# Kernel optimization log

Measured on AMD Instinct MI355X. Metric: run time of the kernel, lower is better.

The kernel has to match this reference:

```python
import jax, jax.numpy as jnp
import numpy as np

# 20 amino-acid letters and per-residue atom counts (len(struct.atoms) - 1 in the source)
LETTERS = "ARNDCQEGHILKMFPSTWYV"
RES_LEN = {"A": 4, "R": 10, "N": 7, "D": 7, "C": 5, "Q": 8, "E": 8, "G": 3, "H": 9,
           "I": 7, "L": 7, "K": 8, "M": 7, "F": 10, "P": 6, "S": 5, "T": 6, "W": 13,
           "Y": 11, "V": 6}
BATCH = 16
N_RES = 1024       # number of residues (output 'nodes')
ATOM_DIM = 64
AMINO_DIM = 256
INDS = 1           # one trailing (3,) tensor axis


def make_metadata():
    """Deterministic protein sequence + per-letter gather indices (static numpy)."""
    rng = np.random.default_rng(42)
    seq = rng.integers(0, len(LETTERS), size=N_RES)
    lens = np.array([RES_LEN[LETTERS[s]] for s in seq])
    starts = np.concatenate([[0], np.cumsum(lens)[:-1]])  # residue_indices
    atoms = int(lens.sum())
    # group residues by letter: (residue positions, atom gather indices (n_l, L))
    groups = {}
    for li, letter in enumerate(LETTERS):
        pos = np.where(seq == li)[0]
        if len(pos) == 0:
            continue
        L = RES_LEN[letter]
        idx = starts[pos][:, None] + np.arange(L)[None, :]  # (n_l, L)
        groups[letter] = (pos, idx)
    # static row offsets of each letter's weight block inside the flat weight
    offsets, off = {}, 0
    for letter in LETTERS:
        offsets[letter] = off
        off += RES_LEN[letter] * ATOM_DIM
    return atoms, groups, offsets


def setup_inputs() -> dict:
    atoms, groups, offsets = make_metadata()
    key = jax.random.key(0)
    k1, k2 = jax.random.split(key)
    x = jax.random.normal(k1, (BATCH, atoms, ATOM_DIM, 3), dtype=jnp.float32)
    total_rows = sum(RES_LEN[l] for l in LETTERS) * ATOM_DIM  # 147*64 = 9408
    W = jax.random.normal(k2, (total_rows, AMINO_DIM), dtype=jnp.float32)
    # per-expert 1/sqrt(fan_in) init scaling
    scale = np.zeros((total_rows, 1), np.float32)
    for l in LETTERS:
        fan = RES_LEN[l] * ATOM_DIM
        scale[offsets[l]:offsets[l] + fan] = 1.0 / np.sqrt(fan)
    W = W * jnp.asarray(scale)
    return {"x": x, "W_flat": W}


def reference(x, W_flat):
    """x: (B, atoms, D, 3); W_flat: (sum_l L_l*D, amino_dim).
    Equivalent to per-residue slice -> reshape -> per-letter TensLinear -> stack,
    but grouped by letter into batched GEMMs (same math, reordered)."""
    atoms, groups, offsets = make_metadata()
    B = x.shape[0]
    out = jnp.zeros((B, N_RES, AMINO_DIM, 3), dtype=x.dtype)
    for letter, (pos, idx) in groups.items():  # fixed loop over <=20 expert types
        L = RES_LEN[letter]
        fan = L * ATOM_DIM
        g = x[:, idx]                              # (B, n_l, L, D, 3) gather
        g = g.reshape(B, len(pos), fan, 3)         # flatten residue atoms x channels
        Wl = W_flat[offsets[letter]:offsets[letter] + fan]  # (fan, amino_dim)
        y = jnp.einsum("bnki,ko->bnoi", g, Wl)     # (B, n_l, amino_dim, 3)
        out = out.at[:, pos].set(y)                # scatter back into residue order
    return out
```

## Files before the change

### kernel.cpp

```cpp
#include <hip/hip_runtime.h>
#include <hip/hip_bf16.h>
#include <cstdint>
#include <cstddef>

#define NRES 1024
#define NB 16
#define ADIM 64
#define ODIM 256
#define TOTROWS 9408

typedef __bf16 bf16x8 __attribute__((ext_vector_type(8)));
typedef float f32x4 __attribute__((ext_vector_type(4)));

struct Meta {
    uint16_t start[NRES];
    uint8_t  letter[NRES];
    int atoms;
};

constexpr int RES_LEN_A[20] = {4,10,7,7,5,8,8,3,9,7,7,8,7,10,6,5,6,13,11,6};

constexpr uint32_t ss_hash(uint32_t value, uint32_t& hc) {
    value ^= hc;
    hc *= 0x931e8875u;
    value *= hc;
    value ^= value >> 16;
    return value;
}
constexpr uint32_t ss_mix(uint32_t x, uint32_t y) {
    uint32_t r = 0xca01f9ddu * x - 0x4973f715u * y;
    r ^= r >> 16;
    return r;
}

constexpr Meta make_meta() {
    Meta m = {};
    uint32_t pool[4] = {0,0,0,0};
    uint32_t hc = 0x43b0d7e5u;
    pool[0] = ss_hash(42u, hc);
    pool[1] = ss_hash(0u, hc);
    pool[2] = ss_hash(0u, hc);
    pool[3] = ss_hash(0u, hc);
    for (int s = 0; s < 4; ++s)
        for (int d = 0; d < 4; ++d)
            if (s != d) pool[d] = ss_mix(pool[d], ss_hash(pool[s], hc));
    uint32_t hb = 0x8b51f9ddu;
    uint64_t w[8] = {};
    for (int i = 0; i < 8; ++i) {
        uint32_t dv = pool[i & 3] ^ hb;
        hb *= 0x58f38dedu;
        dv *= hb;
        dv ^= dv >> 16;
        w[i] = dv;
    }
    uint64_t s64[4] = {};
    for (int i = 0; i < 4; ++i) s64[i] = w[2*i] | (w[2*i+1] << 32);
    using u128 = unsigned __int128;
    const u128 MULT = ((u128)2549297995355413924ULL << 64) | (u128)4865540595714422341ULL;
    u128 initstate = ((u128)s64[0] << 64) | (u128)s64[1];
    u128 initseq   = ((u128)s64[2] << 64) | (u128)s64[3];
    u128 inc = (initseq << 1) | (u128)1;
    u128 state = inc;
    state += initstate;
    state = state * MULT + inc;
    bool has32 = false;
    uint32_t cached = 0;
    int atoms = 0;
    for (int i = 0; i < NRES; ++i) {
        uint32_t res = 0;
        while (true) {
            uint32_t r32;
            if (has32) { r32 = cached; has32 = false; }
            else {
                state = state * MULT + inc;
                uint64_t hi = (uint64_t)(state >> 64);
                uint64_t lo = (uint64_t)state;
                uint32_t rot = (uint32_t)(state >> 122);
                uint64_t v = hi ^ lo;
                uint64_t o64 = (v >> rot) | (v << ((64u - rot) & 63u));
                cached = (uint32_t)(o64 >> 32);
                has32 = true;
                r32 = (uint32_t)o64;
            }
            uint64_t mm = (uint64_t)r32 * 20ull;
            uint32_t leftover = (uint32_t)mm;
            if (leftover >= 16u) { res = (uint32_t)(mm >> 32); break; }
        }
        m.letter[i] = (uint8_t)res;
        m.start[i] = (uint16_t)atoms;
        atoms += RES_LEN_A[res];
    }
    m.atoms = atoms;
    return m;
}

constexpr Meta H_META = make_meta();

struct LetterTab {
    int woff[21];
    int fan[20];
};
constexpr LetterTab make_tab() {
    LetterTab t = {};
    int off = 0;
    for (int l = 0; l < 20; ++l) {
        t.woff[l] = off;
        t.fan[l] = RES_LEN_A[l] * ADIM;
        off += t.fan[l];
    }
    t.woff[20] = off;
    return t;
}

struct Perm { uint16_t p[NRES]; };
constexpr Perm make_perm() {
    int ord[20];
    for (int i = 0; i < 20; ++i) ord[i] = i;
    for (int a = 0; a < 20; ++a) {
        int best = a;
        for (int j = a + 1; j < 20; ++j)
            if (RES_LEN_A[ord[j]] > RES_LEN_A[ord[best]]) best = j;
        int t = ord[a]; ord[a] = ord[best]; ord[best] = t;
    }
    Perm pr = {};
    int n = 0;
    for (int oi = 0; oi < 20; ++oi) {
        const int l = ord[oi];
        for (int p = 0; p < NRES; ++p)
            if (H_META.letter[p] == l) pr.p[n++] = (uint16_t)p;
    }
    return pr;
}

__constant__ Meta g_meta = make_meta();
__constant__ LetterTab g_tab = make_tab();
__constant__ Perm g_perm = make_perm();

__device__ __bf16 g_Wt[(size_t)TOTROWS * ODIM];

__global__ __launch_bounds__(256) void prep_W_kernel(const float* __restrict__ W) {
    const int tid = threadIdx.x;
    const int b = blockIdx.x * 4 + (tid >> 6);
    const int lane = tid & 63;
    const int l15 = lane & 15;
    const int g4 = lane >> 4;

    int l = 0;
    while (b >= (g_tab.woff[l + 1] >> 1)) ++l;
    const int rel = b - (g_tab.woff[l] >> 1);
    const int c = rel >> 5;
    const int r32 = rel & 31;
    const int h = r32 >> 4;
    const int wv = (r32 >> 2) & 3;
    const int nt = r32 & 3;

    const int n = wv * 64 + nt * 16 + l15;
    const int kg = g_tab.woff[l] + c * 64 + h * 32 + g4 * 8;

    bf16x8 v;
    #pragma unroll
    for (int q = 0; q < 8; ++q)
        v[q] = (__bf16)W[(size_t)(kg + q) * ODIM + n];
    *(bf16x8*)&g_Wt[(size_t)b * 512 + (size_t)(l15 * 4 + g4) * 8] = v;
}

__global__ __launch_bounds__(256) void lin_mfma_kernel(const float* __restrict__ x,
                                                       float* __restrict__ out,
                                                       int atoms) {
    const int p = g_perm.p[blockIdx.x];
    const int letter = g_meta.letter[p];
    const int start = g_meta.start[p];
    const int fan = g_tab.fan[letter];
    const __bf16* wslab = g_Wt + (size_t)g_tab.woff[letter] * ODIM;

    const int tid = threadIdx.x;
    const int lane = tid & 63;
    const int wv = tid >> 6;
    const int l15 = lane & 15;
    const int g4 = lane >> 4;

    __shared__ __align__(16) __bf16 As[2][48][72];

    const float* xb = x + (size_t)start * 192;
    const size_t bstr = (size_t)atoms * 192;
    const int nc = fan >> 6;

    int bl_[3], r4_[3];
    #pragma unroll
    for (int j = 0; j < 3; ++j) {
        const int e4 = tid + 256 * j;
        bl_[j] = e4 / 48;
        r4_[j] = e4 - bl_[j] * 48;
    }

    f32x4 acc[3][4];
    #pragma unroll
    for (int t = 0; t < 3; ++t)
        #pragma unroll
        for (int nt = 0; nt < 4; ++nt)
            acc[t][nt] = (f32x4){0.f, 0.f, 0.f, 0.f};

    float4 sa0, sa1, sa2;
    float4 sb0, sb1, sb2;

    auto LOADX = [&](int cc, float4& v0, float4& v1, float4& v2) {
        const size_t koff = (size_t)cc * 192;
        v0 = *(const float4*)&xb[(size_t)bl_[0] * bstr + koff + (size_t)r4_[0] * 4];
        v1 = *(const float4*)&xb[(size_t)bl_[1] * bstr + koff + (size_t)r4_[1] * 4];
        v2 = *(const float4*)&xb[(size_t)bl_[2] * bstr + koff + (size_t)r4_[2] * 4];
    };

    auto CHUNK = [&](int buf, int cc, float4& v0, float4& v1, float4& v2) {
        const float4 vv[3] = {v0, v1, v2};
        #pragma unroll
        for (int j = 0; j < 3; ++j) {
            const float f[4] = {vv[j].x, vv[j].y, vv[j].z, vv[j].w};
            #pragma unroll
            for (int q = 0; q < 4; ++q) {
                const int r = r4_[j] * 4 + q;
                const int kl = r / 3, i = r - kl * 3;
                As[buf][bl_[j] * 3 + i][kl] = (__bf16)f[q];
            }
        }
        if (cc + 2 < nc) LOADX(cc + 2, v0, v1, v2);
        __syncthreads();

        const __bf16* wchunk = wslab + (size_t)cc * 16384 + (size_t)wv * 2048
                             + (size_t)(l15 * 4 + g4) * 8;
        #pragma unroll
        for (int h = 0; h < 2; ++h) {
            bf16x8 a[3], wf[4];
            #pragma unroll
            for (int t = 0; t < 3; ++t)
                a[t] = *(const bf16x8*)&As[buf][t * 16 + l15][h * 32 + g4 * 8];
            #pragma unroll
            for (int nt = 0; nt < 4; ++nt)
                wf[nt] = *(const bf16x8*)(wchunk + (size_t)h * 8192 + (size_t)nt * 512);
            #pragma unroll
            for (int nt = 0; nt < 4; ++nt)
                #pragma unroll
                for (int t = 0; t < 3; ++t)
                    acc[t][nt] = __builtin_amdgcn_mfma_f32_16x16x32_bf16(a[t], wf[nt], acc[t][nt], 0, 0, 0);
        }
    };

    LOADX(0, sa0, sa1, sa2);
    LOADX(1, sb0, sb1, sb2);
    int c = 0;
    while (true) {
        CHUNK(c & 1, c, sa0, sa1, sa2);
        if (++c == nc) break;
        CHUNK(c & 1, c, sb0, sb1, sb2);
        if (++c == nc) break;
    }

    #pragma unroll
    for (int t = 0; t < 3; ++t)
        #pragma unroll
        for (int reg = 0; reg < 4; ++reg) {
            const int r = t * 16 + g4 * 4 + reg;
            const int bl = r / 3;
            const int i = r - bl * 3;
            #pragma unroll
            for (int nt = 0; nt < 4; ++nt) {
                const int o = wv * 64 + nt * 16 + l15;
                out[(((size_t)bl * NRES + p) * ODIM + o) * 3 + i] = acc[t][nt][reg];
            }
        }
}

extern "C" void kernel_launch(void* const* d_in, const int* in_sizes, int n_in,
                              void* d_out, int out_size, void* d_ws, size_t ws_size,
                              hipStream_t stream) {
    (void)n_in; (void)out_size; (void)d_ws; (void)ws_size;
    const float* x = (const float*)d_in[0];
    const float* W = (const float*)d_in[1];
    float* out = (float*)d_out;
    const int atoms = in_sizes[0] / (NB * ADIM * 3);
    prep_W_kernel<<<TOTROWS / 8, 256, 0, stream>>>(W);
    lin_mfma_kernel<<<NRES, 256, 0, stream>>>(x, out, atoms);
}
```

Before: 53.01 us.

## Use 512-thread blocks and software-pipeline W fragment loads across chunks

Doubles the block to 8 waves, so each wave covers 32 output columns instead of 64, which halves the per-wave accumulators and MFMA work. Weight fragments for the next chunk are now prefetched into registers, and the x tile for the next buffer is committed to LDS after the current compute instead of before it. The aim is to hide global-load latency for both W and x behind the MFMA work and to raise the number of waves per block. In exchange, each A fragment is re-read from LDS by twice as many waves, and the larger blocks may limit occupancy and scheduling.

New measurement: 46.20 us. 1.15x faster.

```diff
diff --git a/kernel.cpp b/kernel.cpp
--- a/kernel.cpp
+++ b/kernel.cpp
@@ -164,7 +164,7 @@
     *(bf16x8*)&g_Wt[(size_t)b * 512 + (size_t)(l15 * 4 + g4) * 8] = v;
 }
 
-__global__ __launch_bounds__(256) void lin_mfma_kernel(const float* __restrict__ x,
+__global__ __launch_bounds__(512) void lin_mfma_kernel(const float* __restrict__ x,
                                                        float* __restrict__ out,
                                                        int atoms) {
     const int p = g_perm.p[blockIdx.x];
@@ -175,7 +175,7 @@
 
     const int tid = threadIdx.x;
     const int lane = tid & 63;
-    const int wv = tid >> 6;
+    const int w8 = tid >> 6;
     const int l15 = lane & 15;
     const int g4 = lane >> 4;
 
@@ -185,73 +185,95 @@
     const size_t bstr = (size_t)atoms * 192;
     const int nc = fan >> 6;
 
-    int bl_[3], r4_[3];
-    #pragma unroll
-    for (int j = 0; j < 3; ++j) {
-        const int e4 = tid + 256 * j;
-        bl_[j] = e4 / 48;
-        r4_[j] = e4 - bl_[j] * 48;
-    }
-
-    f32x4 acc[3][4];
+    const int bl0 = tid / 48, r40 = tid - bl0 * 48;
+    const int e41 = 512 + tid;
+    const int bl1 = e41 / 48, r41 = e41 - bl1 * 48;
+    const bool has1 = (tid < 256);
+
+    const __bf16* wbase = wslab + (size_t)(w8 * 2) * 512 + (size_t)(l15 * 4 + g4) * 8;
+
+    f32x4 acc[3][2];
     #pragma unroll
     for (int t = 0; t < 3; ++t)
         #pragma unroll
-        for (int nt = 0; nt < 4; ++nt)
-            acc[t][nt] = (f32x4){0.f, 0.f, 0.f, 0.f};
-
-    float4 sa0, sa1, sa2;
-    float4 sb0, sb1, sb2;
-
-    auto LOADX = [&](int cc, float4& v0, float4& v1, float4& v2) {
+        for (int n = 0; n < 2; ++n)
+            acc[t][n] = (f32x4){0.f, 0.f, 0.f, 0.f};
+
+    float4 xA0, xA1, xB0, xB1;
+    bf16x8 wP[4], wQ[4];
+
+    auto LOADX = [&](int cc, float4& v0, float4& v1) {
         const size_t koff = (size_t)cc * 192;
-        v0 = *(const float4*)&xb[(size_t)bl_[0] * bstr + koff + (size_t)r4_[0] * 4];
-        v1 = *(const float4*)&xb[(size_t)bl_[1] * bstr + koff + (size_t)r4_[1] * 4];
-        v2 = *(const float4*)&xb[(size_t)bl_[2] * bstr + koff + (size_t)r4_[2] * 4];
+        v0 = *(const float4*)&xb[(size_t)bl0 * bstr + koff + (size_t)r40 * 4];
+        if (has1) v1 = *(const float4*)&xb[(size_t)bl1 * bstr + koff + (size_t)r41 * 4];
     };
-
-    auto CHUNK = [&](int buf, int cc, float4& v0, float4& v1, float4& v2) {
-        const float4 vv[3] = {v0, v1, v2};
-        #pragma unroll
-        for (int j = 0; j < 3; ++j) {
-            const float f[4] = {vv[j].x, vv[j].y, vv[j].z, vv[j].w};
+    auto LOADW = [&](int cc, bf16x8* wf) {
+        const __bf16* wc = wbase + (size_t)cc * 16384;
+        #pragma unroll
+        for (int h = 0; h < 2; ++h)
+            #pragma unroll
+            for (int ntl = 0; ntl < 2; ++ntl)
+                wf[h * 2 + ntl] = *(const bf16x8*)(wc + (size_t)h * 8192 + (size_t)ntl * 512);
+    };
+    auto COMMIT = [&](int buf, const float4& v0, const float4& v1) {
+        const float f0[4] = {v0.x, v0.y, v0.z, v0.w};
+        #pragma unroll
+        for (int q = 0; q < 4; ++q) {
+            const int r = r40 * 4 + q, kl = r / 3, i = r - kl * 3;
+            As[buf][bl0 * 3 + i][kl] = (__bf16)f0[q];
+        }
+        if (has1) {
+            const float f1[4] = {v1.x, v1.y, v1.z, v1.w};
             #pragma unroll
             for (int q = 0; q < 4; ++q) {
-                const int r = r4_[j] * 4 + q;
-                const int kl = r / 3, i = r - kl * 3;
-                As[buf][bl_[j] * 3 + i][kl] = (__bf16)f[q];
+                const int r = r41 * 4 + q, kl = r / 3, i = r - kl * 3;
+                As[buf][bl1 * 3 + i][kl] = (__bf16)f1[q];
             }
         }
-        if (cc + 2 < nc) LOADX(cc + 2, v0, v1, v2);
-        __syncthreads();
-
-        const __bf16* wchunk = wslab + (size_t)cc * 16384 + (size_t)wv * 2048
-                             + (size_t)(l15 * 4 + g4) * 8;
+    };
+    auto COMPUTE = [&](int buf, const bf16x8* wf) {
         #pragma unroll
         for (int h = 0; h < 2; ++h) {
-            bf16x8 a[3], wf[4];
+            bf16x8 a[3];
             #pragma unroll
             for (int t = 0; t < 3; ++t)
                 a[t] = *(const bf16x8*)&As[buf][t * 16 + l15][h * 32 + g4 * 8];
             #pragma unroll
-            for (int nt = 0; nt < 4; ++nt)
-                wf[nt] = *(const bf16x8*)(wchunk + (size_t)h * 8192 + (size_t)nt * 512);
-            #pragma unroll
-            for (int nt = 0; nt < 4; ++nt)
+            for (int ntl = 0; ntl < 2; ++ntl)
                 #pragma unroll
                 for (int t = 0; t < 3; ++t)
-                    acc[t][nt] = __builtin_amdgcn_mfma_f32_16x16x32_bf16(a[t], wf[nt], acc[t][nt], 0, 0, 0);
+                    acc[t][ntl] = __builtin_amdgcn_mfma_f32_16x16x32_bf16(a[t], wf[h * 2 + ntl], acc[t][ntl], 0, 0, 0);
         }
     };
 
-    LOADX(0, sa0, sa1, sa2);
-    LOADX(1, sb0, sb1, sb2);
-    int c = 0;
+    LOADX(0, xA0, xA1);
+    LOADX(1, xB0, xB1);
+    LOADW(0, wP);
+    COMMIT(0, xA0, xA1);
+    if (2 < nc) LOADX(2, xA0, xA1);
+    __syncthreads();
+
+    int c = 0, buf = 0;
     while (true) {
-        CHUNK(c & 1, c, sa0, sa1, sa2);
+        if (c + 1 < nc) LOADW(c + 1, wQ);
+        COMPUTE(buf, wP);
+        if (c + 1 < nc) {
+            COMMIT(buf ^ 1, xB0, xB1);
+            if (c + 3 < nc) LOADX(c + 3, xB0, xB1);
+        }
         if (++c == nc) break;
-        CHUNK(c & 1, c, sb0, sb1, sb2);
+        __syncthreads();
+        buf ^= 1;
+
+        if (c + 1 < nc) LOADW(c + 1, wP);
+        COMPUTE(buf, wQ);
+        if (c + 1 < nc) {
+            COMMIT(buf ^ 1, xA0, xA1);
+            if (c + 3 < nc) LOADX(c + 3, xA0, xA1);
+        }
         if (++c == nc) break;
+        __syncthreads();
+        buf ^= 1;
     }
 
     #pragma unroll
@@ -262,9 +284,9 @@
             const int bl = r / 3;
             const int i = r - bl * 3;
             #pragma unroll
-            for (int nt = 0; nt < 4; ++nt) {
-                const int o = wv * 64 + nt * 16 + l15;
-                out[(((size_t)bl * NRES + p) * ODIM + o) * 3 + i] = acc[t][nt][reg];
+            for (int ntl = 0; ntl < 2; ++ntl) {
+                const int o = w8 * 32 + ntl * 16 + l15;
+                out[(((size_t)bl * NRES + p) * ODIM + o) * 3 + i] = acc[t][ntl][reg];
             }
         }
 }
@@ -278,5 +300,5 @@
     float* out = (float*)d_out;
     const int atoms = in_sizes[0] / (NB * ADIM * 3);
     prep_W_kernel<<<TOTROWS / 8, 256, 0, stream>>>(W);
-    lin_mfma_kernel<<<NRES, 256, 0, stream>>>(x, out, atoms);
-}
+    lin_mfma_kernel<<<NRES, 512, 0, stream>>>(x, out, atoms);
+}
```
